# Kernel optimization log

Measured on AMD Instinct MI355X. Metric: run time of the kernel, lower is better.

Reference implementation:

```python
import jax, jax.numpy as jnp
import numpy as np


def setup_inputs() -> dict:
    key = jax.random.key(0)
    kx, kw = jax.random.split(key)
    x = jax.random.normal(kx, (16, 256, 128, 128), dtype=jnp.float32)
    weight = jax.random.normal(kw, (128, 256, 3, 3), dtype=jnp.float32)
    return {"x": x, "weight": weight}


def reference(x, weight):
    # alpha = mean(|W|) per output channel, shape [Cout] (matches E.squeeze())
    alpha = jnp.mean(jnp.abs(weight), axis=(1, 2, 3))
    binary_weight = jnp.sign(weight)
    binary_input = jnp.sign(x)
    out = jax.lax.conv_general_dilated(
        binary_input, binary_weight,
        window_strides=(1, 1),
        padding=((1, 1), (1, 1)),
        dimension_numbers=("NCHW", "OIHW", "NCHW"),
    )  # [N, Cout, H, W] with W == Cout by construction
    # Faithful to torch: `output * alpha` broadcasts alpha[Cout] along the
    # LAST (width) axis, which equals Cout for the chosen shapes.
    return out * alpha
```

## Files before the change

### kernel.cpp

```cpp
#include <hip/hip_runtime.h>
#include <stdint.h>

#define CIN   256
#define COUT  128
#define HH    128
#define WW    128
#define NIMG  16

typedef unsigned long long u64;
typedef unsigned int u32;
typedef unsigned short u16;
typedef u32 u32x2 __attribute__((ext_vector_type(2)));
typedef u32 u32x4 __attribute__((ext_vector_type(4)));
typedef int i32x4 __attribute__((ext_vector_type(4)));
typedef int i32x16 __attribute__((ext_vector_type(16)));
typedef signed char i8;

__global__ __launch_bounds__(256) void pack_x_kernel(const float* __restrict__ x,
                                                     u64* __restrict__ px) {
    int t = blockIdx.x * 256 + threadIdx.x;
    int w = t & (WW - 1);
    int h = (t >> 7) & (HH - 1);
    int n = t >> 14;
    const float* xp = x + (size_t)n * CIN * HH * WW + (size_t)h * WW + w;
    u64 words[4];
#pragma unroll
    for (int wd = 0; wd < 4; ++wd) {
        u64 acc = 0;
#pragma unroll 16
        for (int cc = 0; cc < 64; ++cc) {
            float v = xp[(size_t)(wd * 64 + cc) * (HH * WW)];
            acc |= (u64)(v > 0.0f) << cc;
        }
        words[wd] = acc;
    }
    ulonglong2* o = reinterpret_cast<ulonglong2*>(px + (size_t)t * 4);
    o[0] = make_ulonglong2(words[0], words[1]);
    o[1] = make_ulonglong2(words[2], words[3]);
}

__global__ __launch_bounds__(256) void pack_w_kernel(const float* __restrict__ wt,
                                                     i8* __restrict__ wb,
                                                     float* __restrict__ alpha) {
    int co = blockIdx.x;
    int c  = threadIdx.x;
    int lane = c & 63;
    int word = c >> 6;
    const float* wp = wt + ((size_t)co * CIN + c) * 9;
    float asum = 0.0f;
#pragma unroll
    for (int k = 0; k < 9; ++k) {
        float v = wp[k];
        asum += fabsf(v);
        wb[(size_t)co * 2304 + k * 256 + c] = (v > 0.0f) ? (i8)1 : (i8)-1;
    }
    __shared__ float red[4];
    for (int off = 32; off > 0; off >>= 1) asum += __shfl_down(asum, off);
    if (lane == 0) red[word] = asum;
    __syncthreads();
    if (c == 0) alpha[co] = (red[0] + red[1] + red[2] + red[3]) * (1.0f / 2304.0f);
}

__device__ __forceinline__ i32x4 expand16(u32 v) {
    u32 o0 = __builtin_amdgcn_perm(0x01010101u, 0xFFFFFFFFu,
              ((((v      ) & 15u) * 0x00204081u) & 0x01010101u) << 2);
    u32 o1 = __builtin_amdgcn_perm(0x01010101u, 0xFFFFFFFFu,
              ((((v >>  4) & 15u) * 0x00204081u) & 0x01010101u) << 2);
    u32 o2 = __builtin_amdgcn_perm(0x01010101u, 0xFFFFFFFFu,
              ((((v >>  8) & 15u) * 0x00204081u) & 0x01010101u) << 2);
    u32 o3 = __builtin_amdgcn_perm(0x01010101u, 0xFFFFFFFFu,
              ((((v >> 12) & 15u) * 0x00204081u) & 0x01010101u) << 2);
    i32x4 r = {(int)o0, (int)o1, (int)o2, (int)o3};
    return r;
}

__global__ __launch_bounds__(256, 3) void conv_kernel(const u64* __restrict__ px,
                                                      const i8* __restrict__ wb,
                                                      const float* __restrict__ alpha,
                                                      float* __restrict__ out) {
    __shared__ u16 xlt[3][16][130];
    __shared__ __align__(16) i8 wl[2][128 * 128];
    __shared__ float alds[WW];

    int tid = threadIdx.x;
    int bid = blockIdx.x;
    int h = bid & (HH - 1);
    int n = bid >> 7;

    if (tid < WW) alds[tid] = alpha[tid];

    int sco = tid >> 1, sq = tid & 1;
    u32x4 g0, g1, g2, g3;
    {
        const u32x4* s = reinterpret_cast<const u32x4*>(
            wb + (size_t)sco * 2304 + sq * 64);
        g0 = s[0]; g1 = s[1]; g2 = s[2]; g3 = s[3];
    }

    for (int t = tid; t < 390; t += 256) {
        int r = (t >= 260) ? 2 : ((t >= 130) ? 1 : 0);
        int p = t - r * 130;
        int gh = h - 1 + r;
        u32 bw[8] = {0, 0, 0, 0, 0, 0, 0, 0};
        if ((p >= 1) && (p <= 128) && (gh >= 0) && (gh < HH)) {
            const u32x4* s = reinterpret_cast<const u32x4*>(
                px + (size_t)((n * HH + gh) * WW + (p - 1)) * 4);
            u32x4 a = s[0], b = s[1];
            bw[0] = a.x; bw[1] = a.y; bw[2] = a.z; bw[3] = a.w;
            bw[4] = b.x; bw[5] = b.y; bw[6] = b.z; bw[7] = b.w;
        }
#pragma unroll
        for (int k16 = 0; k16 < 16; ++k16)
            xlt[r][k16][p] = (u16)(bw[k16 >> 1] >> ((k16 & 1) * 16));
    }

    {
        i8* basew = wl[0] + (sco << 7);
        int swzc = (sco & 15) << 3;
        int qo = sq * 64;
        u32x2 p0 = {g0.x, g0.y}, p1 = {g0.z, g0.w};
        u32x2 p2 = {g1.x, g1.y}, p3 = {g1.z, g1.w};
        u32x2 p4 = {g2.x, g2.y}, p5 = {g2.z, g2.w};
        u32x2 p6 = {g3.x, g3.y}, p7 = {g3.z, g3.w};
        *reinterpret_cast<u32x2*>(basew + ((qo + 0)  ^ swzc)) = p0;
        *reinterpret_cast<u32x2*>(basew + ((qo + 8)  ^ swzc)) = p1;
        *reinterpret_cast<u32x2*>(basew + ((qo + 16) ^ swzc)) = p2;
        *reinterpret_cast<u32x2*>(basew + ((qo + 24) ^ swzc)) = p3;
        *reinterpret_cast<u32x2*>(basew + ((qo + 32) ^ swzc)) = p4;
        *reinterpret_cast<u32x2*>(basew + ((qo + 40) ^ swzc)) = p5;
        *reinterpret_cast<u32x2*>(basew + ((qo + 48) ^ swzc)) = p6;
        *reinterpret_cast<u32x2*>(basew + ((qo + 56) ^ swzc)) = p7;
    }
    __syncthreads();

    int lane = tid & 63;
    int wave = tid >> 6;
    int l31 = lane & 31;
    int hi  = lane >> 5;
    int co0  = (wave & 1) * 64;
    int pos0 = (wave >> 1) * 64;

    i32x16 accA0 = {}, accA1 = {}, accB0 = {}, accB1 = {};

    int swzw = (l31 & 15) << 3;

#pragma unroll 1
    for (int ch = 0; ch < 18; ++ch) {
        int nxt = ch + 1;
        if (nxt < 18) {
            const u32x4* s = reinterpret_cast<const u32x4*>(
                wb + (size_t)sco * 2304 + nxt * 128 + sq * 64);
            g0 = s[0]; g1 = s[1]; g2 = s[2]; g3 = s[3];
        }
        int tap = ch >> 1;
        int k16b = (ch & 1) * 8;
        int r   = tap / 3;
        int dwi = tap - r * 3;
        int colA = pos0 + l31 + dwi;
        int colB = colA + 32;
        bool rowOK = (r == 1) || (r == 0 ? (h > 0) : (h < HH - 1));
        int mA = (rowOK && colA >= 1 && colA <= 128) ? -1 : 0;
        int mB = (rowOK && colB >= 1 && colB <= 128) ? -1 : 0;
        i32x4 mvA = {mA, mA, mA, mA};
        i32x4 mvB = {mB, mB, mB, mB};
        const i8* wbuf = wl[ch & 1];
        const i8* wr0 = wbuf + ((co0 + l31) << 7);
        const i8* wr1 = wbuf + ((co0 + 32 + l31) << 7);
#pragma unroll
        for (int ks = 0; ks < 4; ++ks) {
            int k16 = k16b + ks * 2 + hi;
            i32x4 xfA = expand16((u32)xlt[r][k16][colA]) & mvA;
            i32x4 xfB = expand16((u32)xlt[r][k16][colB]) & mvB;
            int kk = ks * 32 + hi * 16;
            u32x2 wa0 = *reinterpret_cast<const u32x2*>(wr0 + (kk ^ swzw));
            u32x2 wa1 = *reinterpret_cast<const u32x2*>(wr0 + ((kk + 8) ^ swzw));
            u32x2 wc0 = *reinterpret_cast<const u32x2*>(wr1 + (kk ^ swzw));
            u32x2 wc1 = *reinterpret_cast<const u32x2*>(wr1 + ((kk + 8) ^ swzw));
            i32x4 wf0 = {(int)wa0.x, (int)wa0.y, (int)wa1.x, (int)wa1.y};
            i32x4 wf1 = {(int)wc0.x, (int)wc0.y, (int)wc1.x, (int)wc1.y};
            accA0 = __builtin_amdgcn_mfma_i32_32x32x32_i8(wf0, xfA, accA0, 0, 0, 0);
            accA1 = __builtin_amdgcn_mfma_i32_32x32x32_i8(wf1, xfA, accA1, 0, 0, 0);
            accB0 = __builtin_amdgcn_mfma_i32_32x32x32_i8(wf0, xfB, accB0, 0, 0, 0);
            accB1 = __builtin_amdgcn_mfma_i32_32x32x32_i8(wf1, xfB, accB1, 0, 0, 0);
        }
        __syncthreads();
        if (nxt < 18) {
            i8* basew = wl[nxt & 1] + (sco << 7);
            int swzc = (sco & 15) << 3;
            int qo = sq * 64;
            u32x2 p0 = {g0.x, g0.y}, p1 = {g0.z, g0.w};
            u32x2 p2 = {g1.x, g1.y}, p3 = {g1.z, g1.w};
            u32x2 p4 = {g2.x, g2.y}, p5 = {g2.z, g2.w};
            u32x2 p6 = {g3.x, g3.y}, p7 = {g3.z, g3.w};
            *reinterpret_cast<u32x2*>(basew + ((qo + 0)  ^ swzc)) = p0;
            *reinterpret_cast<u32x2*>(basew + ((qo + 8)  ^ swzc)) = p1;
            *reinterpret_cast<u32x2*>(basew + ((qo + 16) ^ swzc)) = p2;
            *reinterpret_cast<u32x2*>(basew + ((qo + 24) ^ swzc)) = p3;
            *reinterpret_cast<u32x2*>(basew + ((qo + 32) ^ swzc)) = p4;
            *reinterpret_cast<u32x2*>(basew + ((qo + 40) ^ swzc)) = p5;
            *reinterpret_cast<u32x2*>(basew + ((qo + 48) ^ swzc)) = p6;
            *reinterpret_cast<u32x2*>(basew + ((qo + 56) ^ swzc)) = p7;
            __syncthreads();
        }
    }

#pragma unroll
    for (int half = 0; half < 2; ++half) {
        int wcol = pos0 + half * 32 + l31;
        float aw = alds[wcol];
        i32x16 a0 = half ? accB0 : accA0;
        i32x16 a1 = half ? accB1 : accA1;
#pragma unroll
        for (int reg = 0; reg < 16; ++reg) {
            int rr = (reg & 3) + 8 * (reg >> 2) + 4 * hi;
            out[((size_t)(n * COUT + co0 + rr) * HH + h) * WW + wcol] =
                (float)a0[reg] * aw;
            out[((size_t)(n * COUT + co0 + 32 + rr) * HH + h) * WW + wcol] =
                (float)a1[reg] * aw;
        }
    }
}

extern "C" void kernel_launch(void* const* d_in, const int* in_sizes, int n_in,
                              void* d_out, int out_size, void* d_ws, size_t ws_size,
                              hipStream_t stream) {
    const float* x  = (const float*)d_in[0];
    const float* wt = (const float*)d_in[1];
    float* out = (float*)d_out;

    char* ws = (char*)d_ws;
    const size_t PX_BYTES = (size_t)NIMG * HH * WW * 4 * sizeof(u64);
    const size_t WB_BYTES = (size_t)COUT * 2304;
    const size_t AL_BYTES = 512;
    if (ws_size < PX_BYTES + WB_BYTES + AL_BYTES) return;
    u64*   px    = (u64*)ws;
    i8*    wbuf  = (i8*)(ws + PX_BYTES);
    float* alpha = (float*)(ws + PX_BYTES + WB_BYTES);

    pack_x_kernel<<<NIMG * HH * WW / 256, 256, 0, stream>>>(x, px);
    pack_w_kernel<<<COUT, 256, 0, stream>>>(wt, wbuf, alpha);
    conv_kernel<<<NIMG * HH, 256, 0, stream>>>(px, wbuf, alpha, out);
}
```

Before: 168.7 us.

## Prefetch weights two chunks ahead and drop one barrier per chunk

Weight chunks are now loaded from global memory two chunks ahead into registers, so each load has a full compute iteration to complete before its data is written to LDS. Each iteration writes the next chunk into the opposite buffer right after its MFMAs and issues a single barrier, where there used to be two. With double buffering, the buffer being written was last read in the previous iteration, so the barrier that ended that iteration already protects it. The pipeline is deeper, but register pressure and the correctness of the buffer-reuse ordering become more delicate.

Measured after the change: 167.1 us. No clear change (-0.9%).

```diff
diff --git a/kernel.cpp b/kernel.cpp
--- a/kernel.cpp
+++ b/kernel.cpp
@@ -90,6 +90,11 @@
     if (tid < WW) alds[tid] = alpha[tid];
 
     int sco = tid >> 1, sq = tid & 1;
+    int swzc = (sco & 15) << 3;
+    i8* wbase0 = wl[0] + (sco << 7);
+    i8* wbase1 = wl[1] + (sco << 7);
+    int qo = sq * 64;
+
     u32x4 g0, g1, g2, g3;
     {
         const u32x4* s = reinterpret_cast<const u32x4*>(
@@ -115,21 +120,23 @@
     }
 
     {
-        i8* basew = wl[0] + (sco << 7);
-        int swzc = (sco & 15) << 3;
-        int qo = sq * 64;
         u32x2 p0 = {g0.x, g0.y}, p1 = {g0.z, g0.w};
         u32x2 p2 = {g1.x, g1.y}, p3 = {g1.z, g1.w};
         u32x2 p4 = {g2.x, g2.y}, p5 = {g2.z, g2.w};
         u32x2 p6 = {g3.x, g3.y}, p7 = {g3.z, g3.w};
-        *reinterpret_cast<u32x2*>(basew + ((qo + 0)  ^ swzc)) = p0;
-        *reinterpret_cast<u32x2*>(basew + ((qo + 8)  ^ swzc)) = p1;
-        *reinterpret_cast<u32x2*>(basew + ((qo + 16) ^ swzc)) = p2;
-        *reinterpret_cast<u32x2*>(basew + ((qo + 24) ^ swzc)) = p3;
-        *reinterpret_cast<u32x2*>(basew + ((qo + 32) ^ swzc)) = p4;
-        *reinterpret_cast<u32x2*>(basew + ((qo + 40) ^ swzc)) = p5;
-        *reinterpret_cast<u32x2*>(basew + ((qo + 48) ^ swzc)) = p6;
-        *reinterpret_cast<u32x2*>(basew + ((qo + 56) ^ swzc)) = p7;
+        *reinterpret_cast<u32x2*>(wbase0 + ((qo + 0)  ^ swzc)) = p0;
+        *reinterpret_cast<u32x2*>(wbase0 + ((qo + 8)  ^ swzc)) = p1;
+        *reinterpret_cast<u32x2*>(wbase0 + ((qo + 16) ^ swzc)) = p2;
+        *reinterpret_cast<u32x2*>(wbase0 + ((qo + 24) ^ swzc)) = p3;
+        *reinterpret_cast<u32x2*>(wbase0 + ((qo + 32) ^ swzc)) = p4;
+        *reinterpret_cast<u32x2*>(wbase0 + ((qo + 40) ^ swzc)) = p5;
+        *reinterpret_cast<u32x2*>(wbase0 + ((qo + 48) ^ swzc)) = p6;
+        *reinterpret_cast<u32x2*>(wbase0 + ((qo + 56) ^ swzc)) = p7;
+    }
+    {
+        const u32x4* s = reinterpret_cast<const u32x4*>(
+            wb + (size_t)sco * 2304 + 128 + sq * 64);
+        g0 = s[0]; g1 = s[1]; g2 = s[2]; g3 = s[3];
     }
     __syncthreads();
 
@@ -146,12 +153,6 @@
 
 #pragma unroll 1
     for (int ch = 0; ch < 18; ++ch) {
-        int nxt = ch + 1;
-        if (nxt < 18) {
-            const u32x4* s = reinterpret_cast<const u32x4*>(
-                wb + (size_t)sco * 2304 + nxt * 128 + sq * 64);
-            g0 = s[0]; g1 = s[1]; g2 = s[2]; g3 = s[3];
-        }
         int tap = ch >> 1;
         int k16b = (ch & 1) * 8;
         int r   = tap / 3;
@@ -183,11 +184,8 @@
             accB0 = __builtin_amdgcn_mfma_i32_32x32x32_i8(wf0, xfB, accB0, 0, 0, 0);
             accB1 = __builtin_amdgcn_mfma_i32_32x32x32_i8(wf1, xfB, accB1, 0, 0, 0);
         }
-        __syncthreads();
-        if (nxt < 18) {
-            i8* basew = wl[nxt & 1] + (sco << 7);
-            int swzc = (sco & 15) << 3;
-            int qo = sq * 64;
+        if (ch < 17) {
+            i8* basew = (ch & 1) ? wbase0 : wbase1;
             u32x2 p0 = {g0.x, g0.y}, p1 = {g0.z, g0.w};
             u32x2 p2 = {g1.x, g1.y}, p3 = {g1.z, g1.w};
             u32x2 p4 = {g2.x, g2.y}, p5 = {g2.z, g2.w};
@@ -200,6 +198,11 @@
             *reinterpret_cast<u32x2*>(basew + ((qo + 40) ^ swzc)) = p5;
             *reinterpret_cast<u32x2*>(basew + ((qo + 48) ^ swzc)) = p6;
             *reinterpret_cast<u32x2*>(basew + ((qo + 56) ^ swzc)) = p7;
+            if (ch < 16) {
+                const u32x4* s = reinterpret_cast<const u32x4*>(
+                    wb + (size_t)sco * 2304 + (ch + 2) * 128 + sq * 64);
+                g0 = s[0]; g1 = s[1]; g2 = s[2]; g3 = s[3];
+            }
             __syncthreads();
         }
     }
```

## Use 0/1 input bits with weight-sum correction and read weights directly from global

Applied to the files above, without the earlier changes.

Input bits are now expanded to 0/1 bytes instead of ±1, and the result is recovered as 2*acc minus a precomputed per-border-pattern weight sum, so the per-element perm and padding masks go away. Weights are stored in an MFMA-fragment-friendly layout and read straight from global/L2 each step, which removes the double-buffered shared weight tile and the per-chunk barriers. Dropping that shared buffer also allows the launch bound to rise from 3 to 4 blocks per CU. The cost is more global/L2 weight traffic per wave and extra pattern-sum work in the weight-packing kernel.

After: 150.2 us. 11.0% less time.

```diff
diff --git a/kernel.cpp b/kernel.cpp
--- a/kernel.cpp
+++ b/kernel.cpp
@@ -10,7 +10,6 @@
 typedef unsigned long long u64;
 typedef unsigned int u32;
 typedef unsigned short u16;
-typedef u32 u32x2 __attribute__((ext_vector_type(2)));
 typedef u32 u32x4 __attribute__((ext_vector_type(4)));
 typedef int i32x4 __attribute__((ext_vector_type(4)));
 typedef int i32x16 __attribute__((ext_vector_type(16)));
@@ -40,46 +39,65 @@
 }
 
 __global__ __launch_bounds__(256) void pack_w_kernel(const float* __restrict__ wt,
-                                                     i8* __restrict__ wb,
+                                                     i8* __restrict__ wg,
+                                                     short* __restrict__ wsum,
                                                      float* __restrict__ alpha) {
     int co = blockIdx.x;
     int c  = threadIdx.x;
     int lane = c & 63;
     int word = c >> 6;
+    __shared__ u64 wsh[9][4];
+    __shared__ int pct[9];
+    __shared__ float red[4];
     const float* wp = wt + ((size_t)co * CIN + c) * 9;
     float asum = 0.0f;
 #pragma unroll
     for (int k = 0; k < 9; ++k) {
         float v = wp[k];
         asum += fabsf(v);
-        wb[(size_t)co * 2304 + k * 256 + c] = (v > 0.0f) ? (i8)1 : (i8)-1;
-    }
-    __shared__ float red[4];
+        u64 m = __ballot(v > 0.0f);
+        if (lane == 0) wsh[k][word] = m;
+        int k16g = k * 16 + (c >> 4);
+        wg[((size_t)k16g * COUT + co) * 16 + (c & 15)] = (v > 0.0f) ? (i8)1 : (i8)-1;
+    }
     for (int off = 32; off > 0; off >>= 1) asum += __shfl_down(asum, off);
     if (lane == 0) red[word] = asum;
     __syncthreads();
+    if (c < 9)
+        pct[c] = __popcll(wsh[c][0]) + __popcll(wsh[c][1]) +
+                 __popcll(wsh[c][2]) + __popcll(wsh[c][3]);
     if (c == 0) alpha[co] = (red[0] + red[1] + red[2] + red[3]) * (1.0f / 2304.0f);
-}
-
-__device__ __forceinline__ i32x4 expand16(u32 v) {
-    u32 o0 = __builtin_amdgcn_perm(0x01010101u, 0xFFFFFFFFu,
-              ((((v      ) & 15u) * 0x00204081u) & 0x01010101u) << 2);
-    u32 o1 = __builtin_amdgcn_perm(0x01010101u, 0xFFFFFFFFu,
-              ((((v >>  4) & 15u) * 0x00204081u) & 0x01010101u) << 2);
-    u32 o2 = __builtin_amdgcn_perm(0x01010101u, 0xFFFFFFFFu,
-              ((((v >>  8) & 15u) * 0x00204081u) & 0x01010101u) << 2);
-    u32 o3 = __builtin_amdgcn_perm(0x01010101u, 0xFFFFFFFFu,
-              ((((v >> 12) & 15u) * 0x00204081u) & 0x01010101u) << 2);
+    __syncthreads();
+    if (c < 9) {
+        int pat = c, ht = pat / 3, wtp = pat % 3;
+        int s = 0;
+#pragma unroll
+        for (int k = 0; k < 9; ++k) {
+            int dh = k / 3 - 1, dw = k % 3 - 1;
+            bool inv = (dh == -1 && ht == 0) || (dh == 1 && ht == 2) ||
+                       (dw == -1 && wtp == 0) || (dw == 1 && wtp == 2);
+            if (!inv) s += 2 * pct[k] - 256;
+        }
+        wsum[pat * COUT + co] = (short)s;
+    }
+}
+
+__device__ __forceinline__ i32x4 spread16(u32 v) {
+    u32 o0 = (((v      ) & 15u) * 0x00204081u) & 0x01010101u;
+    u32 o1 = (((v >>  4) & 15u) * 0x00204081u) & 0x01010101u;
+    u32 o2 = (((v >>  8) & 15u) * 0x00204081u) & 0x01010101u;
+    u32 o3 = (((v >> 12) & 15u) * 0x00204081u) & 0x01010101u;
     i32x4 r = {(int)o0, (int)o1, (int)o2, (int)o3};
     return r;
 }
 
-__global__ __launch_bounds__(256, 3) void conv_kernel(const u64* __restrict__ px,
-                                                      const i8* __restrict__ wb,
+__global__ __launch_bounds__(256, 4) void conv_kernel(const u64* __restrict__ px,
+                                                      const i8* __restrict__ wg,
+                                                      const short* __restrict__ wsum,
                                                       const float* __restrict__ alpha,
                                                       float* __restrict__ out) {
     __shared__ u16 xlt[3][16][130];
-    __shared__ __align__(16) i8 wl[2][128 * 128];
+    __shared__ short wsl[9 * COUT];
     __shared__ float alds[WW];
 
     int tid = threadIdx.x;
@@ -88,13 +106,10 @@
     int n = bid >> 7;
 
     if (tid < WW) alds[tid] = alpha[tid];
-
-    int sco = tid >> 1, sq = tid & 1;
-    u32x4 g0, g1, g2, g3;
     {
-        const u32x4* s = reinterpret_cast<const u32x4*>(
-            wb + (size_t)sco * 2304 + sq * 64);
-        g0 = s[0]; g1 = s[1]; g2 = s[2]; g3 = s[3];
+        const u32* s = reinterpret_cast<const u32*>(wsum);
+        u32* d = reinterpret_cast<u32*>(wsl);
+        for (int i = tid; i < 9 * COUT / 2; i += 256) d[i] = s[i];
     }
 
     for (int t = tid; t < 390; t += 256) {
@@ -113,24 +128,6 @@
         for (int k16 = 0; k16 < 16; ++k16)
             xlt[r][k16][p] = (u16)(bw[k16 >> 1] >> ((k16 & 1) * 16));
     }
-
-    {
-        i8* basew = wl[0] + (sco << 7);
-        int swzc = (sco & 15) << 3;
-        int qo = sq * 64;
-        u32x2 p0 = {g0.x, g0.y}, p1 = {g0.z, g0.w};
-        u32x2 p2 = {g1.x, g1.y}, p3 = {g1.z, g1.w};
-        u32x2 p4 = {g2.x, g2.y}, p5 = {g2.z, g2.w};
-        u32x2 p6 = {g3.x, g3.y}, p7 = {g3.z, g3.w};
-        *reinterpret_cast<u32x2*>(basew + ((qo + 0)  ^ swzc)) = p0;
-        *reinterpret_cast<u32x2*>(basew + ((qo + 8)  ^ swzc)) = p1;
-        *reinterpret_cast<u32x2*>(basew + ((qo + 16) ^ swzc)) = p2;
-        *reinterpret_cast<u32x2*>(basew + ((qo + 24) ^ swzc)) = p3;
-        *reinterpret_cast<u32x2*>(basew + ((qo + 32) ^ swzc)) = p4;
-        *reinterpret_cast<u32x2*>(basew + ((qo + 40) ^ swzc)) = p5;
-        *reinterpret_cast<u32x2*>(basew + ((qo + 48) ^ swzc)) = p6;
-        *reinterpret_cast<u32x2*>(basew + ((qo + 56) ^ swzc)) = p7;
-    }
     __syncthreads();
 
     int lane = tid & 63;
@@ -142,81 +139,50 @@
 
     i32x16 accA0 = {}, accA1 = {}, accB0 = {}, accB1 = {};
 
-    int swzw = (l31 & 15) << 3;
-
 #pragma unroll 1
     for (int ch = 0; ch < 18; ++ch) {
-        int nxt = ch + 1;
-        if (nxt < 18) {
-            const u32x4* s = reinterpret_cast<const u32x4*>(
-                wb + (size_t)sco * 2304 + nxt * 128 + sq * 64);
-            g0 = s[0]; g1 = s[1]; g2 = s[2]; g3 = s[3];
-        }
         int tap = ch >> 1;
         int k16b = (ch & 1) * 8;
         int r   = tap / 3;
         int dwi = tap - r * 3;
         int colA = pos0 + l31 + dwi;
         int colB = colA + 32;
-        bool rowOK = (r == 1) || (r == 0 ? (h > 0) : (h < HH - 1));
-        int mA = (rowOK && colA >= 1 && colA <= 128) ? -1 : 0;
-        int mB = (rowOK && colB >= 1 && colB <= 128) ? -1 : 0;
-        i32x4 mvA = {mA, mA, mA, mA};
-        i32x4 mvB = {mB, mB, mB, mB};
-        const i8* wbuf = wl[ch & 1];
-        const i8* wr0 = wbuf + ((co0 + l31) << 7);
-        const i8* wr1 = wbuf + ((co0 + 32 + l31) << 7);
+        int k16gb = tap * 16 + k16b;
 #pragma unroll
         for (int ks = 0; ks < 4; ++ks) {
             int k16 = k16b + ks * 2 + hi;
-            i32x4 xfA = expand16((u32)xlt[r][k16][colA]) & mvA;
-            i32x4 xfB = expand16((u32)xlt[r][k16][colB]) & mvB;
-            int kk = ks * 32 + hi * 16;
-            u32x2 wa0 = *reinterpret_cast<const u32x2*>(wr0 + (kk ^ swzw));
-            u32x2 wa1 = *reinterpret_cast<const u32x2*>(wr0 + ((kk + 8) ^ swzw));
-            u32x2 wc0 = *reinterpret_cast<const u32x2*>(wr1 + (kk ^ swzw));
-            u32x2 wc1 = *reinterpret_cast<const u32x2*>(wr1 + ((kk + 8) ^ swzw));
-            i32x4 wf0 = {(int)wa0.x, (int)wa0.y, (int)wa1.x, (int)wa1.y};
-            i32x4 wf1 = {(int)wc0.x, (int)wc0.y, (int)wc1.x, (int)wc1.y};
+            i32x4 xfA = spread16((u32)xlt[r][k16][colA]);
+            i32x4 xfB = spread16((u32)xlt[r][k16][colB]);
+            int k16g = k16gb + ks * 2 + hi;
+            const i32x4* wp = reinterpret_cast<const i32x4*>(
+                wg + ((size_t)k16g * COUT) * 16);
+            i32x4 wf0 = wp[co0 + l31];
+            i32x4 wf1 = wp[co0 + 32 + l31];
             accA0 = __builtin_amdgcn_mfma_i32_32x32x32_i8(wf0, xfA, accA0, 0, 0, 0);
             accA1 = __builtin_amdgcn_mfma_i32_32x32x32_i8(wf1, xfA, accA1, 0, 0, 0);
             accB0 = __builtin_amdgcn_mfma_i32_32x32x32_i8(wf0, xfB, accB0, 0, 0, 0);
             accB1 = __builtin_amdgcn_mfma_i32_32x32x32_i8(wf1, xfB, accB1, 0, 0, 0);
         }
-        __syncthreads();
-        if (nxt < 18) {
-            i8* basew = wl[nxt & 1] + (sco << 7);
-            int swzc = (sco & 15) << 3;
-            int qo = sq * 64;
-            u32x2 p0 = {g0.x, g0.y}, p1 = {g0.z, g0.w};
-            u32x2 p2 = {g1.x, g1.y}, p3 = {g1.z, g1.w};
-            u32x2 p4 = {g2.x, g2.y}, p5 = {g2.z, g2.w};
-            u32x2 p6 = {g3.x, g3.y}, p7 = {g3.z, g3.w};
-            *reinterpret_cast<u32x2*>(basew + ((qo + 0)  ^ swzc)) = p0;
-            *reinterpret_cast<u32x2*>(basew + ((qo + 8)  ^ swzc)) = p1;
-            *reinterpret_cast<u32x2*>(basew + ((qo + 16) ^ swzc)) = p2;
-            *reinterpret_cast<u32x2*>(basew + ((qo + 24) ^ swzc)) = p3;
-            *reinterpret_cast<u32x2*>(basew + ((qo + 32) ^ swzc)) = p4;
-            *reinterpret_cast<u32x2*>(basew + ((qo + 40) ^ swzc)) = p5;
-            *reinterpret_cast<u32x2*>(basew + ((qo + 48) ^ swzc)) = p6;
-            *reinterpret_cast<u32x2*>(basew + ((qo + 56) ^ swzc)) = p7;
-            __syncthreads();
-        }
-    }
-
+    }
+
+    int hpat = (h == 0) ? 0 : ((h == HH - 1) ? 2 : 1);
 #pragma unroll
     for (int half = 0; half < 2; ++half) {
         int wcol = pos0 + half * 32 + l31;
         float aw = alds[wcol];
+        int wpat = (wcol == 0) ? 0 : ((wcol == WW - 1) ? 2 : 1);
+        const short* wsp = &wsl[(hpat * 3 + wpat) * COUT];
         i32x16 a0 = half ? accB0 : accA0;
         i32x16 a1 = half ? accB1 : accA1;
 #pragma unroll
         for (int reg = 0; reg < 16; ++reg) {
             int rr = (reg & 3) + 8 * (reg >> 2) + 4 * hi;
-            out[((size_t)(n * COUT + co0 + rr) * HH + h) * WW + wcol] =
-                (float)a0[reg] * aw;
-            out[((size_t)(n * COUT + co0 + 32 + rr) * HH + h) * WW + wcol] =
-                (float)a1[reg] * aw;
+            int coa = co0 + rr;
+            int cob = co0 + 32 + rr;
+            out[((size_t)(n * COUT + coa) * HH + h) * WW + wcol] =
+                (float)(2 * a0[reg] - (int)wsp[coa]) * aw;
+            out[((size_t)(n * COUT + cob) * HH + h) * WW + wcol] =
+                (float)(2 * a1[reg] - (int)wsp[cob]) * aw;
         }
     }
 }
@@ -230,14 +196,16 @@
 
     char* ws = (char*)d_ws;
     const size_t PX_BYTES = (size_t)NIMG * HH * WW * 4 * sizeof(u64);
-    const size_t WB_BYTES = (size_t)COUT * 2304;
+    const size_t WG_BYTES = (size_t)144 * COUT * 16;
+    const size_t WS_BYTES = (size_t)9 * COUT * sizeof(short);
     const size_t AL_BYTES = 512;
-    if (ws_size < PX_BYTES + WB_BYTES + AL_BYTES) return;
+    if (ws_size < PX_BYTES + WG_BYTES + WS_BYTES + AL_BYTES) return;
     u64*   px    = (u64*)ws;
-    i8*    wbuf  = (i8*)(ws + PX_BYTES);
-    float* alpha = (float*)(ws + PX_BYTES + WB_BYTES);
+    i8*    wg    = (i8*)(ws + PX_BYTES);
+    short* wsum  = (short*)(ws + PX_BYTES + WG_BYTES);
+    float* alpha = (float*)(ws + PX_BYTES + WG_BYTES + WS_BYTES);
 
     pack_x_kernel<<<NIMG * HH * WW / 256, 256, 0, stream>>>(x, px);
-    pack_w_kernel<<<COUT, 256, 0, stream>>>(wt, wbuf, alpha);
-    conv_kernel<<<NIMG * HH, 256, 0, stream>>>(px, wbuf, alpha, out);
-}
+    pack_w_kernel<<<COUT, 256, 0, stream>>>(wt, wg, wsum, alpha);
+    conv_kernel<<<NIMG * HH, 256, 0, stream>>>(px, wg, wsum, alpha, out);
+}
```
